# Performance work log

Hardware: AMD Instinct MI355X
Metric: run time of the kernel (lower is better)

## Reference

```python
import jax, jax.numpy as jnp
from jax import lax
import numpy as np

B, S, I, H, O = 4096, 32, 16, 32, 1


def setup_inputs() -> dict:
    key = jax.random.key(0)
    ks = jax.random.split(key, 20)
    sc = 0.1
    inp = {
        "x": jax.random.normal(ks[0], (B, S, I), dtype=jnp.float32),
        "t": jnp.sort(jax.random.uniform(ks[1], (B, S), dtype=jnp.float32), axis=1),
        "gru_Wih": jax.random.normal(ks[2], (3 * H, I), dtype=jnp.float32) * sc,
        "gru_Whh": jax.random.normal(ks[3], (3 * H, H), dtype=jnp.float32) * sc,
        "gru_bih": jax.random.normal(ks[4], (3 * H,), dtype=jnp.float32) * sc,
        "gru_bhh": jax.random.normal(ks[5], (3 * H,), dtype=jnp.float32) * sc,
        "ode_W1": jax.random.normal(ks[6], (64, H), dtype=jnp.float32) * sc,
        "ode_b1": jax.random.normal(ks[7], (64,), dtype=jnp.float32) * sc,
        "ode_W2": jax.random.normal(ks[8], (32, 64), dtype=jnp.float32) * sc,
        "ode_b2": jax.random.normal(ks[9], (32,), dtype=jnp.float32) * sc,
        "ode_W3": jax.random.normal(ks[10], (H, 32), dtype=jnp.float32) * sc,
        "ode_b3": jax.random.normal(ks[11], (H,), dtype=jnp.float32) * sc,
        "fc_W1": jax.random.normal(ks[12], (64, H), dtype=jnp.float32) * sc,
        "fc_b1": jax.random.normal(ks[13], (64,), dtype=jnp.float32) * sc,
        "fc_W2": jax.random.normal(ks[14], (O, 64), dtype=jnp.float32) * sc,
        "fc_b2": jax.random.normal(ks[15], (O,), dtype=jnp.float32) * sc,
        "time_divs": 5,
    }
    return inp


def _forward(x, t, gru_Wih, gru_Whh, gru_bih, gru_bhh,
             ode_W1, ode_b1, ode_W2, ode_b2, ode_W3, ode_b3,
             fc_W1, fc_b1, fc_W2, fc_b2, time_divs):
    n_sub = int(time_divs) - 1  # intervals of the t_eval linspace grid

    def gru_cell(x_t, h):
        gi = x_t @ gru_Wih.T + gru_bih
        gh = h @ gru_Whh.T + gru_bhh
        i_r, i_z, i_n = jnp.split(gi, 3, axis=-1)
        h_r, h_z, h_n = jnp.split(gh, 3, axis=-1)
        r = jax.nn.sigmoid(i_r + h_r)
        z = jax.nn.sigmoid(i_z + h_z)
        n = jnp.tanh(i_n + r * h_n)
        return (1.0 - z) * n + z * h

    def ode_f(y):  # ODEFunc MLP: H -> 64 -> 32 -> H
        h1 = jax.nn.relu(y @ ode_W1.T + ode_b1)
        h2 = jax.nn.relu(h1 @ ode_W2.T + ode_b2)
        return h2 @ ode_W3.T + ode_b3

    def dopri5_step(y, dt):  # dt: (B,1); 5th-order Dormand-Prince step
        k1 = ode_f(y)
        k2 = ode_f(y + dt * (0.2 * k1))
        k3 = ode_f(y + dt * (3 / 40 * k1 + 9 / 40 * k2))
        k4 = ode_f(y + dt * (44 / 45 * k1 - 56 / 15 * k2 + 32 / 9 * k3))
        k5 = ode_f(y + dt * (19372 / 6561 * k1 - 25360 / 2187 * k2
                             + 64448 / 6561 * k3 - 212 / 729 * k4))
        k6 = ode_f(y + dt * (9017 / 3168 * k1 - 355 / 33 * k2 + 46732 / 5247 * k3
                             + 49 / 176 * k4 - 5103 / 18656 * k5))
        return y + dt * (35 / 384 * k1 + 500 / 1113 * k3 + 125 / 192 * k4
                         - 2187 / 6784 * k5 + 11 / 84 * k6)

    def step(carry, inputs):
        h, _ = carry
        x_t, dt = inputs           # x_t: (B,I), dt: (B,)
        out = gru_cell(x_t, h)     # GRU output (also candidate next hidden)
        hi = out
        ddt = (dt / n_sub)[:, None]
        for _ in range(n_sub):     # small fixed substep count, unrolled
            hi = dopri5_step(hi, ddt)
        return (hi, out), None

    bsz = x.shape[0]
    x_seq = jnp.swapaxes(x, 0, 1)[:-1]        # (S-1, B, I)
    dts = (t[:, 1:] - t[:, :-1]).T            # (S-1, B)
    h0 = jnp.zeros((bsz, gru_Whh.shape[1]), dtype=x.dtype)
    (_, out), _ = lax.scan(step, (h0, h0), (x_seq, dts))
    y = jax.nn.relu(out @ fc_W1.T + fc_b1) @ fc_W2.T + fc_b2
    return y


def reference(x, t, gru_Wih, gru_Whh, gru_bih, gru_bhh,
              ode_W1, ode_b1, ode_W2, ode_b2, ode_W3, ode_b3,
              fc_W1, fc_b1, fc_W2, fc_b2, time_divs):
    return _forward(x, t, gru_Wih, gru_Whh, gru_bih, gru_bhh,
                    ode_W1, ode_b1, ode_W2, ode_b2, ode_W3, ode_b3,
                    fc_W1, fc_b1, fc_W2, fc_b2, time_divs)
```

## Files before the change

### kernel.cpp

```cpp
#include <hip/hip_runtime.h>
#include <hip/hip_bf16.h>

#define NB 4096
#define NS 32
#define NI 16
#define NH 32

typedef float f32x2 __attribute__((ext_vector_type(2)));

__device__ __forceinline__ void fence() {
    __builtin_amdgcn_wave_barrier();
    asm volatile("s_waitcnt lgkmcnt(0)" ::: "memory");
    __builtin_amdgcn_wave_barrier();
}

__device__ __forceinline__ float xhsum(float x) {
    auto p = __builtin_amdgcn_permlane32_swap(
        (int)__float_as_uint(x), (int)__float_as_uint(x), false, false);
    return __uint_as_float((unsigned)p[0]) + __uint_as_float((unsigned)p[1]);
}

__device__ __forceinline__ f32x2 pkfma(f32x2 a, f32x2 b, f32x2 c) {
    return __builtin_elementwise_fma(a, b, c);
}

__global__ void __launch_bounds__(256)
__attribute__((amdgpu_waves_per_eu(2, 2)))
odernn_kernel(
    const float* __restrict__ x,
    const float* __restrict__ t,
    const float* __restrict__ gWih,
    const float* __restrict__ gWhh,
    const float* __restrict__ gbih,
    const float* __restrict__ gbhh,
    const float* __restrict__ oW1,
    const float* __restrict__ ob1,
    const float* __restrict__ oW2,
    const float* __restrict__ ob2,
    const float* __restrict__ oW3,
    const float* __restrict__ ob3,
    const float* __restrict__ fW1,
    const float* __restrict__ fb1,
    const float* __restrict__ fW2,
    const float* __restrict__ fb2,
    float* __restrict__ outp)
{
    const int tid  = threadIdx.x;
    const int lane = tid & 63;
    const int wid  = tid >> 6;
    const int b    = blockIdx.x * 4 + wid;
    const int r    = lane & 31;
    const int hf   = lane >> 5;

    __shared__ float sWr[48 * 32];
    __shared__ float sWz[48 * 32];
    __shared__ float sWnh[32 * 32];
    __shared__ float sWni[16 * 32];
    __shared__ __align__(16) float buf[4][64];

    for (int i = tid; i < 48 * 32; i += 256) {
        int c = i >> 5, r0 = i & 31;
        sWr[i] = (c < 16) ? gWih[r0 * 16 + c]        : gWhh[r0 * 32 + (c - 16)];
        sWz[i] = (c < 16) ? gWih[(32 + r0) * 16 + c] : gWhh[(32 + r0) * 32 + (c - 16)];
    }
    for (int i = tid; i < 32 * 32; i += 256) {
        int c = i >> 5, r0 = i & 31;
        sWnh[i] = gWhh[(64 + r0) * 32 + c];
    }
    for (int i = tid; i < 16 * 32; i += 256) {
        int c = i >> 5, r0 = i & 31;
        sWni[i] = gWih[(64 + r0) * 16 + c];
    }
    __syncthreads();

    float* bufw = buf[wid];
    const float4* bb = reinterpret_cast<const float4*>(bufw);

    f32x2 w1_0, w1_1, w1_2, w1_3, w1_4, w1_5, w1_6, w1_7,
          w1_8, w1_9, w1_10, w1_11, w1_12, w1_13, w1_14, w1_15;
    f32x2 w2_0, w2_1, w2_2, w2_3, w2_4, w2_5, w2_6, w2_7,
          w2_8, w2_9, w2_10, w2_11, w2_12, w2_13, w2_14, w2_15;
    f32x2 w3_0, w3_1, w3_2, w3_3, w3_4, w3_5, w3_6, w3_7;
    {
        const float4* p1 = reinterpret_cast<const float4*>(oW1) + lane * 8;
        float4 v;
#define LD2(i, dA, dB) { v = p1[i]; dA = f32x2{v.x, v.y}; dB = f32x2{v.z, v.w}; }
        LD2(0, w1_0,  w1_1)  LD2(1, w1_2,  w1_3)
        LD2(2, w1_4,  w1_5)  LD2(3, w1_6,  w1_7)
        LD2(4, w1_8,  w1_9)  LD2(5, w1_10, w1_11)
        LD2(6, w1_12, w1_13) LD2(7, w1_14, w1_15)
#undef LD2
        const float4* p2 = reinterpret_cast<const float4*>(oW2) + r * 16 + hf * 8;
#define LD2(i, dA, dB) { v = p2[i]; dA = f32x2{v.x, v.y}; dB = f32x2{v.z, v.w}; }
        LD2(0, w2_0,  w2_1)  LD2(1, w2_2,  w2_3)
        LD2(2, w2_4,  w2_5)  LD2(3, w2_6,  w2_7)
        LD2(4, w2_8,  w2_9)  LD2(5, w2_10, w2_11)
        LD2(6, w2_12, w2_13) LD2(7, w2_14, w2_15)
#undef LD2
        const float4* p3 = reinterpret_cast<const float4*>(oW3) + r * 8 + hf * 4;
#define LD2(i, dA, dB) { v = p3[i]; dA = f32x2{v.x, v.y}; dB = f32x2{v.z, v.w}; }
        LD2(0, w3_0, w3_1)  LD2(1, w3_2, w3_3)
        LD2(2, w3_4, w3_5)  LD2(3, w3_6, w3_7)
#undef LD2
    }
    const float b1r = ob1[lane];
    const float b2r = ob2[r];
    const float b3r = ob3[r];

    const float brr = gbih[r]      + gbhh[r];
    const float bzz = gbih[32 + r] + gbhh[32 + r];
    const float bin = gbih[64 + r];
    const float bhn = gbhh[64 + r];

    const float* wrp  = &sWr[(hf * 24) * 32 + r];
    const float* wzp  = &sWz[(hf * 24) * 32 + r];
    const float* wnhp = &sWnh[(hf * 16) * 32 + r];
    const float* wnip = &sWni[r];

    auto ode_f = [&](float yv) -> float {
        bufw[hf * 32 + r] = yv;
        fence();
        f32x2 acc1 = f32x2{b1r, 0.0f};
#define S1(kk, wA, wB) { float4 c = bb[kk]; \
        acc1 = pkfma(wA, f32x2{c.x, c.y}, acc1); \
        acc1 = pkfma(wB, f32x2{c.z, c.w}, acc1); }
        S1(0, w1_0,  w1_1)  S1(1, w1_2,  w1_3)
        S1(2, w1_4,  w1_5)  S1(3, w1_6,  w1_7)
        S1(4, w1_8,  w1_9)  S1(5, w1_10, w1_11)
        S1(6, w1_12, w1_13) S1(7, w1_14, w1_15)
#undef S1
        float a1 = fmaxf(acc1.x + acc1.y, 0.0f);
        bufw[lane] = a1;
        fence();
        f32x2 acc2 = f32x2{0.0f, 0.0f};
        const int o2 = hf * 8;
#define S2(kk, wA, wB) { float4 c = bb[o2 + kk]; \
        acc2 = pkfma(wA, f32x2{c.x, c.y}, acc2); \
        acc2 = pkfma(wB, f32x2{c.z, c.w}, acc2); }
        S2(0, w2_0,  w2_1)  S2(1, w2_2,  w2_3)
        S2(2, w2_4,  w2_5)  S2(3, w2_6,  w2_7)
        S2(4, w2_8,  w2_9)  S2(5, w2_10, w2_11)
        S2(6, w2_12, w2_13) S2(7, w2_14, w2_15)
#undef S2
        float a2 = fmaxf(xhsum(acc2.x + acc2.y) + b2r, 0.0f);
        bufw[hf * 32 + r] = a2;
        fence();
        f32x2 acc3 = f32x2{0.0f, 0.0f};
        const int o3 = hf * 4;
#define S3(kk, wA, wB) { float4 c = bb[o3 + kk]; \
        acc3 = pkfma(wA, f32x2{c.x, c.y}, acc3); \
        acc3 = pkfma(wB, f32x2{c.z, c.w}, acc3); }
        S3(0, w3_0, w3_1)  S3(1, w3_2, w3_3)
        S3(2, w3_4, w3_5)  S3(3, w3_6, w3_7)
#undef S3
        return xhsum(acc3.x + acc3.y) + b3r;
    };

    float hv = 0.0f;
    float outv = 0.0f;

    #pragma unroll 1
    for (int s = 0; s < NS - 1; ++s) {
        const float* xrow = x + ((size_t)b * NS + s) * NI;
        if (hf == 0) {
            bufw[16 + r] = hv;
        } else {
            bufw[r & 15] = xrow[r & 15];
        }
        fence();

        float ar = 0.0f, az = 0.0f;
        #pragma unroll
        for (int kk = 0; kk < 6; ++kk) {
            float4 c = bb[hf*6 + kk];
            ar = fmaf(wrp[(4*kk  )*32], c.x, ar); ar = fmaf(wrp[(4*kk+1)*32], c.y, ar);
            ar = fmaf(wrp[(4*kk+2)*32], c.z, ar); ar = fmaf(wrp[(4*kk+3)*32], c.w, ar);
            az = fmaf(wzp[(4*kk  )*32], c.x, az); az = fmaf(wzp[(4*kk+1)*32], c.y, az);
            az = fmaf(wzp[(4*kk+2)*32], c.z, az); az = fmaf(wzp[(4*kk+3)*32], c.w, az);
        }
        float in_ = 0.0f, hn = 0.0f;
        #pragma unroll
        for (int kk = 0; kk < 4; ++kk) {
            float4 c = bb[kk];
            in_ = fmaf(wnip[(4*kk  )*32], c.x, in_); in_ = fmaf(wnip[(4*kk+1)*32], c.y, in_);
            in_ = fmaf(wnip[(4*kk+2)*32], c.z, in_); in_ = fmaf(wnip[(4*kk+3)*32], c.w, in_);
        }
        #pragma unroll
        for (int kk = 0; kk < 4; ++kk) {
            float4 c = bb[4 + hf*4 + kk];
            hn = fmaf(wnhp[(4*kk  )*32], c.x, hn); hn = fmaf(wnhp[(4*kk+1)*32], c.y, hn);
            hn = fmaf(wnhp[(4*kk+2)*32], c.z, hn); hn = fmaf(wnhp[(4*kk+3)*32], c.w, hn);
        }
        ar = xhsum(ar) + brr;
        az = xhsum(az) + bzz;
        hn = xhsum(hn) + bhn;
        in_ += bin;

        float rg = 1.0f / (1.0f + __expf(-ar));
        float zg = 1.0f / (1.0f + __expf(-az));
        float ng = tanhf(fmaf(rg, hn, in_));
        outv = (1.0f - zg) * ng + zg * hv;

        hv = outv;
        if (s < NS - 2) {
            const float t0 = t[(size_t)b * NS + s];
            const float t1 = t[(size_t)b * NS + s + 1];
            const float ddt = (t1 - t0) * 0.25f;
            float hi = outv;
            #pragma unroll 1
            for (int sub = 0; sub < 4; ++sub) {
                float k1 = ode_f(hi);
                float k2 = ode_f(fmaf(ddt, 0.2f * k1, hi));
                float k3 = ode_f(fmaf(ddt, fmaf((float)(9.0/40.0), k2, (float)(3.0/40.0) * k1), hi));
                float k4 = ode_f(fmaf(ddt,
                        fmaf((float)(32.0/9.0), k3,
                        fmaf(-(float)(56.0/15.0), k2, (float)(44.0/45.0) * k1)), hi));
                float k5 = ode_f(fmaf(ddt,
                        fmaf(-(float)(212.0/729.0), k4,
                        fmaf((float)(64448.0/6561.0), k3,
                        fmaf(-(float)(25360.0/2187.0), k2, (float)(19372.0/6561.0) * k1))), hi));
                float k6 = ode_f(fmaf(ddt,
                        fmaf(-(float)(5103.0/18656.0), k5,
                        fmaf((float)(49.0/176.0), k4,
                        fmaf((float)(46732.0/5247.0), k3,
                        fmaf(-(float)(355.0/33.0), k2, (float)(9017.0/3168.0) * k1)))), hi));
                hi = fmaf(ddt,
                        fmaf((float)(11.0/84.0), k6,
                        fmaf(-(float)(2187.0/6784.0), k5,
                        fmaf((float)(125.0/192.0), k4,
                        fmaf((float)(500.0/1113.0), k3, (float)(35.0/384.0) * k1)))), hi);
            }
            hv = hi;
        }
    }

    bufw[hf * 32 + r] = outv;
    fence();
    f32x2 acc = f32x2{fb1[lane], 0.0f};
    {
        const float4* fw = reinterpret_cast<const float4*>(fW1) + lane * 8;
        #pragma unroll
        for (int kk = 0; kk < 8; ++kk) {
            float4 wv = fw[kk];
            float4 c  = bb[kk];
            acc = pkfma(f32x2{wv.x, wv.y}, f32x2{c.x, c.y}, acc);
            acc = pkfma(f32x2{wv.z, wv.w}, f32x2{c.z, c.w}, acc);
        }
    }
    float a = fmaxf(acc.x + acc.y, 0.0f);
    float p = a * fW2[lane];
    #pragma unroll
    for (int m = 1; m < 64; m <<= 1) p += __shfl_xor(p, m, 64);
    if (lane == 0) outp[b] = p + fb2[0];
}

extern "C" void kernel_launch(void* const* d_in, const int* in_sizes, int n_in,
                              void* d_out, int out_size, void* d_ws, size_t ws_size,
                              hipStream_t stream) {
    (void)in_sizes; (void)n_in; (void)d_ws; (void)ws_size; (void)out_size;
    odernn_kernel<<<dim3(NB / 4), dim3(256), 0, stream>>>(
        (const float*)d_in[0],  (const float*)d_in[1],
        (const float*)d_in[2],  (const float*)d_in[3],
        (const float*)d_in[4],  (const float*)d_in[5],
        (const float*)d_in[6],  (const float*)d_in[7],
        (const float*)d_in[8],  (const float*)d_in[9],
        (const float*)d_in[10], (const float*)d_in[11],
        (const float*)d_in[12], (const float*)d_in[13],
        (const float*)d_in[14], (const float*)d_in[15],
        (float*)d_out);
}
```

Baseline: 749.6 us.

## Process two batch elements per wave to interleave independent recurrences

Each wavefront now carries two batch rows through the GRU and the Dormand-Prince substeps together, with separate LDS buffers and interleaved FMA chains. Weight loads from LDS and registers, and each LDS fence, are shared across both rows. The grid is halved, which reduces the number of waves available to hide latency and increases register pressure.

```diff
diff --git a/kernel.cpp b/kernel.cpp
--- a/kernel.cpp
+++ b/kernel.cpp
@@ -48,7 +48,8 @@
     const int tid  = threadIdx.x;
     const int lane = tid & 63;
     const int wid  = tid >> 6;
-    const int b    = blockIdx.x * 4 + wid;
+    const int b0   = blockIdx.x * 8 + wid * 2;
+    const int b1   = b0 + 1;
     const int r    = lane & 31;
     const int hf   = lane >> 5;
 
@@ -56,7 +57,7 @@
     __shared__ float sWz[48 * 32];
     __shared__ float sWnh[32 * 32];
     __shared__ float sWni[16 * 32];
-    __shared__ __align__(16) float buf[4][64];
+    __shared__ __align__(16) float buf[4][2][64];
 
     for (int i = tid; i < 48 * 32; i += 256) {
         int c = i >> 5, r0 = i & 31;
@@ -73,8 +74,10 @@
     }
     __syncthreads();
 
-    float* bufw = buf[wid];
-    const float4* bb = reinterpret_cast<const float4*>(bufw);
+    float* bufw0 = buf[wid][0];
+    float* bufw1 = buf[wid][1];
+    const float4* bb0 = reinterpret_cast<const float4*>(bufw0);
+    const float4* bb1 = reinterpret_cast<const float4*>(bufw1);
 
     f32x2 w1_0, w1_1, w1_2, w1_3, w1_4, w1_5, w1_6, w1_7,
           w1_8, w1_9, w1_10, w1_11, w1_12, w1_13, w1_14, w1_15;
@@ -117,148 +120,212 @@
     const float* wnhp = &sWnh[(hf * 16) * 32 + r];
     const float* wnip = &sWni[r];
 
-    auto ode_f = [&](float yv) -> float {
-        bufw[hf * 32 + r] = yv;
+    auto ode_f2 = [&](float y0, float y1, float& o0, float& o1) {
+        bufw0[hf * 32 + r] = y0;
+        bufw1[hf * 32 + r] = y1;
         fence();
-        f32x2 acc1 = f32x2{b1r, 0.0f};
-#define S1(kk, wA, wB) { float4 c = bb[kk]; \
-        acc1 = pkfma(wA, f32x2{c.x, c.y}, acc1); \
-        acc1 = pkfma(wB, f32x2{c.z, c.w}, acc1); }
+        f32x2 p0 = f32x2{b1r, 0.0f}, p1a = f32x2{b1r, 0.0f};
+#define S1(kk, wA, wB) { float4 c0 = bb0[kk]; float4 c1 = bb1[kk]; \
+        p0  = pkfma(wA, f32x2{c0.x, c0.y}, p0);  \
+        p0  = pkfma(wB, f32x2{c0.z, c0.w}, p0);  \
+        p1a = pkfma(wA, f32x2{c1.x, c1.y}, p1a); \
+        p1a = pkfma(wB, f32x2{c1.z, c1.w}, p1a); }
         S1(0, w1_0,  w1_1)  S1(1, w1_2,  w1_3)
         S1(2, w1_4,  w1_5)  S1(3, w1_6,  w1_7)
         S1(4, w1_8,  w1_9)  S1(5, w1_10, w1_11)
         S1(6, w1_12, w1_13) S1(7, w1_14, w1_15)
 #undef S1
-        float a1 = fmaxf(acc1.x + acc1.y, 0.0f);
-        bufw[lane] = a1;
+        float a1_0 = fmaxf(p0.x + p0.y, 0.0f);
+        float a1_1 = fmaxf(p1a.x + p1a.y, 0.0f);
+        bufw0[lane] = a1_0;
+        bufw1[lane] = a1_1;
         fence();
-        f32x2 acc2 = f32x2{0.0f, 0.0f};
+        f32x2 q0 = f32x2{0.0f, 0.0f}, q1 = f32x2{0.0f, 0.0f};
         const int o2 = hf * 8;
-#define S2(kk, wA, wB) { float4 c = bb[o2 + kk]; \
-        acc2 = pkfma(wA, f32x2{c.x, c.y}, acc2); \
-        acc2 = pkfma(wB, f32x2{c.z, c.w}, acc2); }
+#define S2(kk, wA, wB) { float4 c0 = bb0[o2 + kk]; float4 c1 = bb1[o2 + kk]; \
+        q0 = pkfma(wA, f32x2{c0.x, c0.y}, q0); \
+        q0 = pkfma(wB, f32x2{c0.z, c0.w}, q0); \
+        q1 = pkfma(wA, f32x2{c1.x, c1.y}, q1); \
+        q1 = pkfma(wB, f32x2{c1.z, c1.w}, q1); }
         S2(0, w2_0,  w2_1)  S2(1, w2_2,  w2_3)
         S2(2, w2_4,  w2_5)  S2(3, w2_6,  w2_7)
         S2(4, w2_8,  w2_9)  S2(5, w2_10, w2_11)
         S2(6, w2_12, w2_13) S2(7, w2_14, w2_15)
 #undef S2
-        float a2 = fmaxf(xhsum(acc2.x + acc2.y) + b2r, 0.0f);
-        bufw[hf * 32 + r] = a2;
+        float a2_0 = fmaxf(xhsum(q0.x + q0.y) + b2r, 0.0f);
+        float a2_1 = fmaxf(xhsum(q1.x + q1.y) + b2r, 0.0f);
+        bufw0[hf * 32 + r] = a2_0;
+        bufw1[hf * 32 + r] = a2_1;
         fence();
-        f32x2 acc3 = f32x2{0.0f, 0.0f};
+        f32x2 s0 = f32x2{0.0f, 0.0f}, s1 = f32x2{0.0f, 0.0f};
         const int o3 = hf * 4;
-#define S3(kk, wA, wB) { float4 c = bb[o3 + kk]; \
-        acc3 = pkfma(wA, f32x2{c.x, c.y}, acc3); \
-        acc3 = pkfma(wB, f32x2{c.z, c.w}, acc3); }
+#define S3(kk, wA, wB) { float4 c0 = bb0[o3 + kk]; float4 c1 = bb1[o3 + kk]; \
+        s0 = pkfma(wA, f32x2{c0.x, c0.y}, s0); \
+        s0 = pkfma(wB, f32x2{c0.z, c0.w}, s0); \
+        s1 = pkfma(wA, f32x2{c1.x, c1.y}, s1); \
+        s1 = pkfma(wB, f32x2{c1.z, c1.w}, s1); }
         S3(0, w3_0, w3_1)  S3(1, w3_2, w3_3)
         S3(2, w3_4, w3_5)  S3(3, w3_6, w3_7)
 #undef S3
-        return xhsum(acc3.x + acc3.y) + b3r;
+        o0 = xhsum(s0.x + s0.y) + b3r;
+        o1 = xhsum(s1.x + s1.y) + b3r;
     };
 
-    float hv = 0.0f;
-    float outv = 0.0f;
+    float hv0 = 0.0f, hv1 = 0.0f;
+    float outv0 = 0.0f, outv1 = 0.0f;
 
     #pragma unroll 1
     for (int s = 0; s < NS - 1; ++s) {
-        const float* xrow = x + ((size_t)b * NS + s) * NI;
+        const float* xrow0 = x + ((size_t)b0 * NS + s) * NI;
+        const float* xrow1 = x + ((size_t)b1 * NS + s) * NI;
         if (hf == 0) {
-            bufw[16 + r] = hv;
+            bufw0[16 + r] = hv0;
+            bufw1[16 + r] = hv1;
         } else {
-            bufw[r & 15] = xrow[r & 15];
+            bufw0[r & 15] = xrow0[r & 15];
+            bufw1[r & 15] = xrow1[r & 15];
         }
         fence();
 
-        float ar = 0.0f, az = 0.0f;
+        float ar0 = 0.f, ar1 = 0.f, az0 = 0.f, az1 = 0.f;
         #pragma unroll
         for (int kk = 0; kk < 6; ++kk) {
-            float4 c = bb[hf*6 + kk];
-            ar = fmaf(wrp[(4*kk  )*32], c.x, ar); ar = fmaf(wrp[(4*kk+1)*32], c.y, ar);
-            ar = fmaf(wrp[(4*kk+2)*32], c.z, ar); ar = fmaf(wrp[(4*kk+3)*32], c.w, ar);
-            az = fmaf(wzp[(4*kk  )*32], c.x, az); az = fmaf(wzp[(4*kk+1)*32], c.y, az);
-            az = fmaf(wzp[(4*kk+2)*32], c.z, az); az = fmaf(wzp[(4*kk+3)*32], c.w, az);
-        }
-        float in_ = 0.0f, hn = 0.0f;
+            float4 c0 = bb0[hf*6 + kk];
+            float4 c1 = bb1[hf*6 + kk];
+            float w;
+            w = wrp[(4*kk  )*32]; ar0 = fmaf(w, c0.x, ar0); ar1 = fmaf(w, c1.x, ar1);
+            w = wrp[(4*kk+1)*32]; ar0 = fmaf(w, c0.y, ar0); ar1 = fmaf(w, c1.y, ar1);
+            w = wrp[(4*kk+2)*32]; ar0 = fmaf(w, c0.z, ar0); ar1 = fmaf(w, c1.z, ar1);
+            w = wrp[(4*kk+3)*32]; ar0 = fmaf(w, c0.w, ar0); ar1 = fmaf(w, c1.w, ar1);
+            w = wzp[(4*kk  )*32]; az0 = fmaf(w, c0.x, az0); az1 = fmaf(w, c1.x, az1);
+            w = wzp[(4*kk+1)*32]; az0 = fmaf(w, c0.y, az0); az1 = fmaf(w, c1.y, az1);
+            w = wzp[(4*kk+2)*32]; az0 = fmaf(w, c0.z, az0); az1 = fmaf(w, c1.z, az1);
+            w = wzp[(4*kk+3)*32]; az0 = fmaf(w, c0.w, az0); az1 = fmaf(w, c1.w, az1);
+        }
+        float in0 = 0.f, in1 = 0.f, hn0 = 0.f, hn1 = 0.f;
         #pragma unroll
         for (int kk = 0; kk < 4; ++kk) {
-            float4 c = bb[kk];
-            in_ = fmaf(wnip[(4*kk  )*32], c.x, in_); in_ = fmaf(wnip[(4*kk+1)*32], c.y, in_);
-            in_ = fmaf(wnip[(4*kk+2)*32], c.z, in_); in_ = fmaf(wnip[(4*kk+3)*32], c.w, in_);
+            float4 c0 = bb0[kk];
+            float4 c1 = bb1[kk];
+            float w;
+            w = wnip[(4*kk  )*32]; in0 = fmaf(w, c0.x, in0); in1 = fmaf(w, c1.x, in1);
+            w = wnip[(4*kk+1)*32]; in0 = fmaf(w, c0.y, in0); in1 = fmaf(w, c1.y, in1);
+            w = wnip[(4*kk+2)*32]; in0 = fmaf(w, c0.z, in0); in1 = fmaf(w, c1.z, in1);
+            w = wnip[(4*kk+3)*32]; in0 = fmaf(w, c0.w, in0); in1 = fmaf(w, c1.w, in1);
         }
         #pragma unroll
         for (int kk = 0; kk < 4; ++kk) {
-            float4 c = bb[4 + hf*4 + kk];
-            hn = fmaf(wnhp[(4*kk  )*32], c.x, hn); hn = fmaf(wnhp[(4*kk+1)*32], c.y, hn);
-            hn = fmaf(wnhp[(4*kk+2)*32], c.z, hn); hn = fmaf(wnhp[(4*kk+3)*32], c.w, hn);
-        }
-        ar = xhsum(ar) + brr;
-        az = xhsum(az) + bzz;
-        hn = xhsum(hn) + bhn;
-        in_ += bin;
-
-        float rg = 1.0f / (1.0f + __expf(-ar));
-        float zg = 1.0f / (1.0f + __expf(-az));
-        float ng = tanhf(fmaf(rg, hn, in_));
-        outv = (1.0f - zg) * ng + zg * hv;
-
-        hv = outv;
+            float4 c0 = bb0[4 + hf*4 + kk];
+            float4 c1 = bb1[4 + hf*4 + kk];
+            float w;
+            w = wnhp[(4*kk  )*32]; hn0 = fmaf(w, c0.x, hn0); hn1 = fmaf(w, c1.x, hn1);
+            w = wnhp[(4*kk+1)*32]; hn0 = fmaf(w, c0.y, hn0); hn1 = fmaf(w, c1.y, hn1);
+            w = wnhp[(4*kk+2)*32]; hn0 = fmaf(w, c0.z, hn0); hn1 = fmaf(w, c1.z, hn1);
+            w = wnhp[(4*kk+3)*32]; hn0 = fmaf(w, c0.w, hn0); hn1 = fmaf(w, c1.w, hn1);
+        }
+        ar0 = xhsum(ar0) + brr;  ar1 = xhsum(ar1) + brr;
+        az0 = xhsum(az0) + bzz;  az1 = xhsum(az1) + bzz;
+        hn0 = xhsum(hn0) + bhn;  hn1 = xhsum(hn1) + bhn;
+        in0 += bin;              in1 += bin;
+
+        float rg0 = 1.0f / (1.0f + __expf(-ar0));
+        float rg1 = 1.0f / (1.0f + __expf(-ar1));
+        float zg0 = 1.0f / (1.0f + __expf(-az0));
+        float zg1 = 1.0f / (1.0f + __expf(-az1));
+        float ng0 = tanhf(fmaf(rg0, hn0, in0));
+        float ng1 = tanhf(fmaf(rg1, hn1, in1));
+        outv0 = (1.0f - zg0) * ng0 + zg0 * hv0;
+        outv1 = (1.0f - zg1) * ng1 + zg1 * hv1;
+
+        hv0 = outv0;
+        hv1 = outv1;
         if (s < NS - 2) {
-            const float t0 = t[(size_t)b * NS + s];
-            const float t1 = t[(size_t)b * NS + s + 1];
-            const float ddt = (t1 - t0) * 0.25f;
-            float hi = outv;
+            const float ddt0 = (t[(size_t)b0 * NS + s + 1] - t[(size_t)b0 * NS + s]) * 0.25f;
+            const float ddt1 = (t[(size_t)b1 * NS + s + 1] - t[(size_t)b1 * NS + s]) * 0.25f;
+            float hi0 = outv0, hi1 = outv1;
             #pragma unroll 1
             for (int sub = 0; sub < 4; ++sub) {
-                float k1 = ode_f(hi);
-                float k2 = ode_f(fmaf(ddt, 0.2f * k1, hi));
-                float k3 = ode_f(fmaf(ddt, fmaf((float)(9.0/40.0), k2, (float)(3.0/40.0) * k1), hi));
-                float k4 = ode_f(fmaf(ddt,
-                        fmaf((float)(32.0/9.0), k3,
-                        fmaf(-(float)(56.0/15.0), k2, (float)(44.0/45.0) * k1)), hi));
-                float k5 = ode_f(fmaf(ddt,
-                        fmaf(-(float)(212.0/729.0), k4,
-                        fmaf((float)(64448.0/6561.0), k3,
-                        fmaf(-(float)(25360.0/2187.0), k2, (float)(19372.0/6561.0) * k1))), hi));
-                float k6 = ode_f(fmaf(ddt,
-                        fmaf(-(float)(5103.0/18656.0), k5,
-                        fmaf((float)(49.0/176.0), k4,
-                        fmaf((float)(46732.0/5247.0), k3,
-                        fmaf(-(float)(355.0/33.0), k2, (float)(9017.0/3168.0) * k1)))), hi));
-                hi = fmaf(ddt,
-                        fmaf((float)(11.0/84.0), k6,
-                        fmaf(-(float)(2187.0/6784.0), k5,
-                        fmaf((float)(125.0/192.0), k4,
-                        fmaf((float)(500.0/1113.0), k3, (float)(35.0/384.0) * k1)))), hi);
+                float k1_0, k1_1, k2_0, k2_1, k3_0, k3_1,
+                      k4_0, k4_1, k5_0, k5_1, k6_0, k6_1;
+                ode_f2(hi0, hi1, k1_0, k1_1);
+                ode_f2(fmaf(ddt0, 0.2f * k1_0, hi0),
+                       fmaf(ddt1, 0.2f * k1_1, hi1), k2_0, k2_1);
+                ode_f2(fmaf(ddt0, fmaf((float)(9.0/40.0), k2_0, (float)(3.0/40.0) * k1_0), hi0),
+                       fmaf(ddt1, fmaf((float)(9.0/40.0), k2_1, (float)(3.0/40.0) * k1_1), hi1),
+                       k3_0, k3_1);
+                ode_f2(fmaf(ddt0, fmaf((float)(32.0/9.0), k3_0,
+                                  fmaf(-(float)(56.0/15.0), k2_0, (float)(44.0/45.0) * k1_0)), hi0),
+                       fmaf(ddt1, fmaf((float)(32.0/9.0), k3_1,
+                                  fmaf(-(float)(56.0/15.0), k2_1, (float)(44.0/45.0) * k1_1)), hi1),
+                       k4_0, k4_1);
+                ode_f2(fmaf(ddt0, fmaf(-(float)(212.0/729.0), k4_0,
+                                  fmaf((float)(64448.0/6561.0), k3_0,
+                                  fmaf(-(float)(25360.0/2187.0), k2_0, (float)(19372.0/6561.0) * k1_0))), hi0),
+                       fmaf(ddt1, fmaf(-(float)(212.0/729.0), k4_1,
+                                  fmaf((float)(64448.0/6561.0), k3_1,
+                                  fmaf(-(float)(25360.0/2187.0), k2_1, (float)(19372.0/6561.0) * k1_1))), hi1),
+                       k5_0, k5_1);
+                ode_f2(fmaf(ddt0, fmaf(-(float)(5103.0/18656.0), k5_0,
+                                  fmaf((float)(49.0/176.0), k4_0,
+                                  fmaf((float)(46732.0/5247.0), k3_0,
+                                  fmaf(-(float)(355.0/33.0), k2_0, (float)(9017.0/3168.0) * k1_0)))), hi0),
+                       fmaf(ddt1, fmaf(-(float)(5103.0/18656.0), k5_1,
+                                  fmaf((float)(49.0/176.0), k4_1,
+                                  fmaf((float)(46732.0/5247.0), k3_1,
+                                  fmaf(-(float)(355.0/33.0), k2_1, (float)(9017.0/3168.0) * k1_1)))), hi1),
+                       k6_0, k6_1);
+                hi0 = fmaf(ddt0, fmaf((float)(11.0/84.0), k6_0,
+                                 fmaf(-(float)(2187.0/6784.0), k5_0,
+                                 fmaf((float)(125.0/192.0), k4_0,
+                                 fmaf((float)(500.0/1113.0), k3_0, (float)(35.0/384.0) * k1_0)))), hi0);
+                hi1 = fmaf(ddt1, fmaf((float)(11.0/84.0), k6_1,
+                                 fmaf(-(float)(2187.0/6784.0), k5_1,
+                                 fmaf((float)(125.0/192.0), k4_1,
+                                 fmaf((float)(500.0/1113.0), k3_1, (float)(35.0/384.0) * k1_1)))), hi1);
             }
-            hv = hi;
-        }
-    }
-
-    bufw[hf * 32 + r] = outv;
+            hv0 = hi0;
+            hv1 = hi1;
+        }
+    }
+
+    bufw0[hf * 32 + r] = outv0;
+    bufw1[hf * 32 + r] = outv1;
     fence();
-    f32x2 acc = f32x2{fb1[lane], 0.0f};
+    f32x2 acc0 = f32x2{fb1[lane], 0.0f};
+    f32x2 acc1h = f32x2{fb1[lane], 0.0f};
     {
         const float4* fw = reinterpret_cast<const float4*>(fW1) + lane * 8;
         #pragma unroll
         for (int kk = 0; kk < 8; ++kk) {
             float4 wv = fw[kk];
-            float4 c  = bb[kk];
-            acc = pkfma(f32x2{wv.x, wv.y}, f32x2{c.x, c.y}, acc);
-            acc = pkfma(f32x2{wv.z, wv.w}, f32x2{c.z, c.w}, acc);
-        }
-    }
-    float a = fmaxf(acc.x + acc.y, 0.0f);
-    float p = a * fW2[lane];
+            float4 c0 = bb0[kk];
+            float4 c1 = bb1[kk];
+            acc0  = pkfma(f32x2{wv.x, wv.y}, f32x2{c0.x, c0.y}, acc0);
+            acc0  = pkfma(f32x2{wv.z, wv.w}, f32x2{c0.z, c0.w}, acc0);
+            acc1h = pkfma(f32x2{wv.x, wv.y}, f32x2{c1.x, c1.y}, acc1h);
+            acc1h = pkfma(f32x2{wv.z, wv.w}, f32x2{c1.z, c1.w}, acc1h);
+        }
+    }
+    float fw2v = fW2[lane];
+    float pa = fmaxf(acc0.x + acc0.y, 0.0f) * fw2v;
+    float pb = fmaxf(acc1h.x + acc1h.y, 0.0f) * fw2v;
     #pragma unroll
-    for (int m = 1; m < 64; m <<= 1) p += __shfl_xor(p, m, 64);
-    if (lane == 0) outp[b] = p + fb2[0];
+    for (int m = 1; m < 64; m <<= 1) {
+        pa += __shfl_xor(pa, m, 64);
+        pb += __shfl_xor(pb, m, 64);
+    }
+    if (lane == 0) {
+        float bias = fb2[0];
+        outp[b0] = pa + bias;
+        outp[b1] = pb + bias;
+    }
 }
 
 extern "C" void kernel_launch(void* const* d_in, const int* in_sizes, int n_in,
                               void* d_out, int out_size, void* d_ws, size_t ws_size,
                               hipStream_t stream) {
     (void)in_sizes; (void)n_in; (void)d_ws; (void)ws_size; (void)out_size;
-    odernn_kernel<<<dim3(NB / 4), dim3(256), 0, stream>>>(
+    odernn_kernel<<<dim3(NB / 8), dim3(256), 0, stream>>>(
         (const float*)d_in[0],  (const float*)d_in[1],
         (const float*)d_in[2],  (const float*)d_in[3],
         (const float*)d_in[4],  (const float*)d_in[5],
```

New measurement: 692.8 us (median of 2 runs). 1.08x faster.
